# Optimization experiments

Measured on AMD Instinct MI355X. Metric: run time of the kernel, lower is better.

The kernel has to match this reference:

```python
import jax, jax.numpy as jnp
import numpy as np

N = 100_000      # nodes
E = 1_600_000    # directed edges (before self-loops)
F_IN = 128       # input node features
H = 4            # attention heads
C = 64           # hidden channels (concat=False -> heads averaged)
NEG_SLOPE = 0.2
BN_EPS = 1e-5


def setup_inputs() -> dict:
    key = jax.random.key(0)
    ks = jax.random.split(key, 16)
    s = 0.05
    return {
        "x": jax.random.normal(ks[0], (N, F_IN), dtype=jnp.float32),
        "edge_index": jax.random.randint(ks[1], (2, E), 0, N, dtype=jnp.int64),
        # GAT layer params: layer 0 has F_IN inputs, layers 1..2 have C inputs
        "W0": jax.random.normal(ks[2], (F_IN, H * C), dtype=jnp.float32) * s,
        "Wl": jax.random.normal(ks[3], (2, C, H * C), dtype=jnp.float32) * s,
        "att_src": jax.random.normal(ks[4], (3, H, C), dtype=jnp.float32) * s,
        "att_dst": jax.random.normal(ks[5], (3, H, C), dtype=jnp.float32) * s,
        "conv_bias": jnp.zeros((3, C), dtype=jnp.float32),
        # BatchNorm1d (inference: running stats)
        "bn_gamma": jnp.ones((3, C), dtype=jnp.float32),
        "bn_beta": jnp.zeros((3, C), dtype=jnp.float32),
        "bn_mean": jax.random.normal(ks[6], (3, C), dtype=jnp.float32) * 0.1,
        "bn_var": jax.random.uniform(ks[7], (3, C), dtype=jnp.float32, minval=0.5, maxval=1.5),
        # MLP head
        "lin1_w": jax.random.normal(ks[8], (C, C // 2), dtype=jnp.float32) * s,
        "lin1_b": jnp.zeros((C // 2,), dtype=jnp.float32),
        "lin2_w": jax.random.normal(ks[9], (C // 2, 1), dtype=jnp.float32) * s,
        "lin2_b": jnp.zeros((1,), dtype=jnp.float32),
    }


def _gat_layer(x, src, dst, W, a_src, a_dst, bias):
    # x: [N, Fin] -> h: [N, H, C]
    h = (x @ W).reshape(-1, H, C)
    # per-node attention logits, gathered per edge: [Etot, H]
    e_src = jnp.einsum("nhc,hc->nh", h, a_src)
    e_dst = jnp.einsum("nhc,hc->nh", h, a_dst)
    e = jax.nn.leaky_relu(e_src[src] + e_dst[dst], NEG_SLOPE)
    # softmax over incoming edges of each target node (self-loops guarantee non-empty)
    e_max = jax.ops.segment_max(e, dst, num_segments=N)
    w = jnp.exp(e - e_max[dst])                              # [Etot, H]
    denom = jax.ops.segment_sum(w, dst, num_segments=N)      # [N, H]
    # weighted scatter-add of gathered source features
    msg = h[src] * w[:, :, None]                             # [Etot, H, C]
    out = jax.ops.segment_sum(msg, dst, num_segments=N)      # [N, H, C]
    out = out / denom[:, :, None]
    return out.mean(axis=1) + bias                           # concat=False -> head mean


def reference(x, edge_index, W0, Wl, att_src, att_dst, conv_bias,
              bn_gamma, bn_beta, bn_mean, bn_var,
              lin1_w, lin1_b, lin2_w, lin2_b):
    # add self-loops (PyG GATConv default)
    loop = jnp.arange(N, dtype=edge_index.dtype)
    src = jnp.concatenate([edge_index[0], loop])
    dst = jnp.concatenate([edge_index[1], loop])

    Ws = [W0, Wl[0], Wl[1]]
    for l in range(3):
        x = _gat_layer(x, src, dst, Ws[l], att_src[l], att_dst[l], conv_bias[l])
        x = (x - bn_mean[l]) * (bn_gamma[l] / jnp.sqrt(bn_var[l] + BN_EPS)) + bn_beta[l]
        x = jax.nn.relu(x)  # dropout is identity in inference

    x = jax.nn.relu(x @ lin1_w + lin1_b)
    x = x @ lin2_w + lin2_b
    return x.squeeze(-1)
```

## Files before the change

### kernel.cpp

```cpp
#include <hip/hip_runtime.h>
#include <hip/hip_bf16.h>
#include <cstdint>

#define N_NODES 100000
#define N_EDGES 1600000
#define N_TOT   1700000
#define HEADS   4
#define CH      64
#define HC      256
#define NEG     0.2f
#define BNEPS   1e-5f
#define NPART   8
#define PART_N  12500
#define CHUNK_E 16384

typedef __attribute__((ext_vector_type(8))) short short8;
typedef __attribute__((ext_vector_type(4))) float f32x4;
typedef __attribute__((ext_vector_type(2))) float f32x2;

static __device__ __forceinline__ float lrelu(float x) {
    return x > 0.f ? x : NEG * x;
}
static __device__ __forceinline__ unsigned short f2bf(float f) {
    unsigned int u = __float_as_uint(f);
    unsigned int r = (u + 0x7fffu + ((u >> 16) & 1u)) >> 16;
    return (unsigned short)r;
}
static __device__ __forceinline__ float bflo(unsigned int v) { return __uint_as_float(v << 16); }
static __device__ __forceinline__ float bfhi(unsigned int v) { return __uint_as_float(v & 0xffff0000u); }

__global__ void convert_hist_k(const void* ei,
                               int* __restrict__ src32, int* __restrict__ dst32,
                               int* __restrict__ counts) {
    const int* e32 = (const int*)ei;
    int l = threadIdx.x & 63;
    unsigned long long b = __ballot(e32[2 * l + 1] == 0);
    int is64 = (__popcll(b) >= 48) ? 1 : 0;

    int e = blockIdx.x * 256 + threadIdx.x;
    if (e >= N_TOT) return;
    int s, d;
    if (e < N_EDGES) {
        if (is64) {
            s = (int)((const long long*)ei)[e];
            d = (int)((const long long*)ei)[(long long)N_EDGES + e];
        } else {
            s = ((const int*)ei)[e];
            d = ((const int*)ei)[N_EDGES + e];
        }
    } else { int v = e - N_EDGES; s = v; d = v; }
    src32[e] = s; dst32[e] = d;
    atomicAdd(&counts[d], 1);
}

__global__ void scan_block(const int* in, int* out, int* bsum) {
    __shared__ int sm[256];
    int t = threadIdx.x;
    int i = blockIdx.x * 256 + t;
    int v = (i < N_NODES) ? in[i] : 0;
    int acc = v;
    sm[t] = v; __syncthreads();
    for (int d = 1; d < 256; d <<= 1) {
        int add = (t >= d) ? sm[t - d] : 0;
        __syncthreads();
        acc += add; sm[t] = acc;
        __syncthreads();
    }
    if (i < N_NODES) out[i] = acc - v;
    if (t == 255) bsum[blockIdx.x] = acc;
}

__global__ void scan_bsum(int* bsum, int nb) {
    __shared__ int sm[512];
    int t = threadIdx.x;
    int v = (t < nb) ? bsum[t] : 0;
    int acc = v;
    sm[t] = v; __syncthreads();
    for (int d = 1; d < 512; d <<= 1) {
        int add = (t >= d) ? sm[t - d] : 0;
        __syncthreads();
        acc += add; sm[t] = acc;
        __syncthreads();
    }
    if (t < nb) bsum[t] = acc - v;
}

__global__ void scan_add(int* off, const int* bsum, int* fill) {
    int i = blockIdx.x * 256 + threadIdx.x;
    if (i < N_NODES) {
        int v = off[i] + bsum[blockIdx.x];
        off[i] = v; fill[i] = v;
    }
    if (i == 0) off[N_NODES] = N_TOT;
}

__global__ void scatter_part_k(const int* __restrict__ src32, const int* __restrict__ dst32,
                               int* __restrict__ fill, int* __restrict__ csr) {
    int part = blockIdx.x & (NPART - 1), chunk = blockIdx.x / NPART;
    int lo = part * PART_N, hi = lo + PART_N;
    int base = chunk * CHUNK_E;
    int end = min(base + CHUNK_E, N_TOT);
    for (int i = base + threadIdx.x; i < end; i += 256) {
        int d = dst32[i];
        if (d >= lo && d < hi) {
            int s = src32[i];
            int pos = atomicAdd(&fill[d], 1);
            csr[pos] = s;
        }
    }
}

template<int K, bool ABF16>
__global__ __launch_bounds__(256) void gemm_mfma_k(const void* __restrict__ Ain,
                                                   const float* __restrict__ Wf,
                                                   const float* __restrict__ as,
                                                   const float* __restrict__ ad,
                                                   unsigned short* __restrict__ hb,
                                                   float* __restrict__ es,
                                                   float* __restrict__ ed, int ntiles) {
    __shared__ __align__(16) unsigned short Bs[256 * K];
    __shared__ __align__(16) unsigned short As[64 * K];
    int t = threadIdx.x;

    for (int idx4 = t; idx4 < K * 64; idx4 += 256) {
        int k = idx4 >> 6;
        int c = (idx4 & 63) * 4;
        float4 wv = *(const float4*)(Wf + (size_t)k * HC + c);
        Bs[((c + 0) * K + k) ^ (((c + 0) & 7) << 3)] = f2bf(wv.x);
        Bs[((c + 1) * K + k) ^ (((c + 1) & 7) << 3)] = f2bf(wv.y);
        Bs[((c + 2) * K + k) ^ (((c + 2) & 7) << 3)] = f2bf(wv.z);
        Bs[((c + 3) * K + k) ^ (((c + 3) & 7) << 3)] = f2bf(wv.w);
    }

    int w = t >> 6, lane = t & 63;
    int c16 = lane & 15, kg = lane >> 4;
    int swz = (c16 & 7) << 3;
    float asv[4], adv[4];
    #pragma unroll
    for (int ct = 0; ct < 4; ++ct) {
        asv[ct] = as[w * 64 + ct * 16 + c16];
        adv[ct] = ad[w * 64 + ct * 16 + c16];
    }
    __syncthreads();

    for (int tile = blockIdx.x; tile < ntiles; tile += gridDim.x) {
        int bm = tile * 64;
        #pragma unroll
        for (int i = 0; i < (64 * K / 8) / 256; ++i) {
            int cidx = i * 256 + t;
            int row = cidx / (K / 8);
            int ks = (cidx % (K / 8)) * 8;
            int grow = bm + row;
            uint4 pk = make_uint4(0, 0, 0, 0);
            if (grow < N_NODES) {
                if (ABF16) {
                    pk = *(const uint4*)((const unsigned short*)Ain + (size_t)grow * K + ks);
                } else {
                    const float* Af = (const float*)Ain + (size_t)grow * K + ks;
                    float4 v0 = *(const float4*)Af;
                    float4 v1 = *(const float4*)(Af + 4);
                    pk.x = (unsigned)f2bf(v0.x) | ((unsigned)f2bf(v0.y) << 16);
                    pk.y = (unsigned)f2bf(v0.z) | ((unsigned)f2bf(v0.w) << 16);
                    pk.z = (unsigned)f2bf(v1.x) | ((unsigned)f2bf(v1.y) << 16);
                    pk.w = (unsigned)f2bf(v1.z) | ((unsigned)f2bf(v1.w) << 16);
                }
            }
            *(uint4*)(&As[(row * K + ks) ^ ((row & 7) << 3)]) = pk;
        }
        __syncthreads();

        f32x4 acc[4][4];
        #pragma unroll
        for (int i = 0; i < 4; ++i)
            #pragma unroll
            for (int j = 0; j < 4; ++j) acc[i][j] = (f32x4)(0.f);

        #pragma unroll
        for (int kc = 0; kc < K / 32; ++kc) {
            int ko = kc * 32 + kg * 8;
            short8 af[4], bf[4];
            #pragma unroll
            for (int rs = 0; rs < 4; ++rs)
                af[rs] = *(const short8*)(&As[((16 * rs + c16) * K + ko) ^ swz]);
            #pragma unroll
            for (int ct = 0; ct < 4; ++ct) {
                int col = w * 64 + ct * 16 + c16;
                bf[ct] = *(const short8*)(&Bs[(col * K + ko) ^ swz]);
            }
            #pragma unroll
            for (int rs = 0; rs < 4; ++rs)
                #pragma unroll
                for (int ct = 0; ct < 4; ++ct)
                    acc[rs][ct] = __builtin_amdgcn_mfma_f32_16x16x32_bf16(af[rs], bf[ct], acc[rs][ct], 0, 0, 0);
        }

        #pragma unroll
        for (int rs = 0; rs < 4; ++rs) {
            float esr[4], edr[4];
            #pragma unroll
            for (int reg = 0; reg < 4; ++reg) {
                float s = 0.f, d = 0.f;
                #pragma unroll
                for (int ct = 0; ct < 4; ++ct) {
                    s += acc[rs][ct][reg] * asv[ct];
                    d += acc[rs][ct][reg] * adv[ct];
                }
                #pragma unroll
                for (int sh = 1; sh < 16; sh <<= 1) {
                    s += __shfl_xor(s, sh);
                    d += __shfl_xor(d, sh);
                }
                esr[reg] = s; edr[reg] = d;
            }
            if (c16 == 0) {
                int r0 = bm + rs * 16 + kg * 4;
                #pragma unroll
                for (int reg = 0; reg < 4; ++reg) {
                    if (r0 + reg < N_NODES) {
                        es[(size_t)(r0 + reg) * 4 + w] = esr[reg];
                        ed[(size_t)(r0 + reg) * 4 + w] = edr[reg];
                    }
                }
            }
        }
        __syncthreads();

        #pragma unroll
        for (int rs = 0; rs < 4; ++rs) {
            #pragma unroll
            for (int ct = 0; ct < 4; ++ct)
                #pragma unroll
                for (int reg = 0; reg < 4; ++reg)
                    As[(kg * 4 + reg) * 256 + w * 64 + ct * 16 + c16] = f2bf(acc[rs][ct][reg]);
            __syncthreads();
            int row16 = t >> 4, cseg = (t & 15) * 16;
            int grow = bm + rs * 16 + row16;
            if (grow < N_NODES) {
                uint4 v0 = *(const uint4*)(&As[row16 * 256 + cseg]);
                uint4 v1 = *(const uint4*)(&As[row16 * 256 + cseg + 8]);
                *(uint4*)(hb + (size_t)grow * HC + cseg) = v0;
                *(uint4*)(hb + (size_t)grow * HC + cseg + 8) = v1;
            }
            __syncthreads();
        }
    }
}

template<bool OUTBF16>
__global__ __launch_bounds__(256) void aggregate_k(const unsigned short* __restrict__ h,
                                                   const float* __restrict__ es,
                                                   const float* __restrict__ ed,
                                                   const int* __restrict__ off,
                                                   const int* __restrict__ csr,
                                                   const float* __restrict__ bias,
                                                   const float* __restrict__ g,
                                                   const float* __restrict__ bb,
                                                   const float* __restrict__ mu,
                                                   const float* __restrict__ var,
                                                   void* __restrict__ xout) {
    __shared__ float wbuf[4][68][4];
    __shared__ int   sbuf[4][68];
    int wv = threadIdx.x >> 6;
    int lane = threadIdx.x & 63;
    int wid = blockIdx.x * 4 + wv;
    if (wid >= N_NODES) return;

    if (lane < 4) {
        sbuf[wv][64 + lane] = 0;
        *(float4*)(&wbuf[wv][64 + lane][0]) = make_float4(0.f, 0.f, 0.f, 0.f);
    }

    int s0 = off[wid], s1 = off[wid + 1];
    float4 edv = *(const float4*)(ed + (size_t)wid * 4);

    int half = lane >> 5;
    int sub  = lane & 31;
    int head = sub >> 3;
    float ds0 = 0.f, ds1 = 0.f, ds2 = 0.f, ds3 = 0.f;
    f32x2 acc2[8];
    #pragma unroll
    for (int i = 0; i < 8; ++i) acc2[i] = (f32x2)(0.f);
    const unsigned short* hsub = h + sub * 8;

    for (int base = s0; base < s1; base += 64) {
        int e = base + lane;
        float w0 = 0.f, w1 = 0.f, w2 = 0.f, w3 = 0.f;
        int s = 0;
        if (e < s1) {
            s = csr[e];
            float4 ev = *(const float4*)(es + (size_t)s * 4);
            w0 = __expf(fminf(lrelu(ev.x + edv.x), 80.f));
            w1 = __expf(fminf(lrelu(ev.y + edv.y), 80.f));
            w2 = __expf(fminf(lrelu(ev.z + edv.z), 80.f));
            w3 = __expf(fminf(lrelu(ev.w + edv.w), 80.f));
        }
        ds0 += w0; ds1 += w1; ds2 += w2; ds3 += w3;
        *(float4*)(&wbuf[wv][lane][0]) = make_float4(w0, w1, w2, w3);
        sbuf[wv][lane] = s;
        asm volatile("" ::: "memory");

        int cnt2 = (min(64, s1 - base) + 1) & ~1;
        int sA = sbuf[wv][half];
        float wA = wbuf[wv][half][head];
        int sB = sbuf[wv][2 + half];
        float wB = wbuf[wv][2 + half][head];
        uint4 hA = *(const uint4*)(hsub + (size_t)sA * HC);
        uint4 hB = *(const uint4*)(hsub + (size_t)sB * HC);
        for (int j = 0; j < cnt2; j += 2) {
            int jn = j + 4 + half;
            int sC = sbuf[wv][jn];
            float wC = wbuf[wv][jn][head];
            uint4 hC = *(const uint4*)(hsub + (size_t)sC * HC);
            f32x2 wp = { wA, wA };
            f32x2 p0 = { bflo(hA.x), bfhi(hA.x) };
            f32x2 p1 = { bflo(hA.y), bfhi(hA.y) };
            f32x2 p2 = { bflo(hA.z), bfhi(hA.z) };
            f32x2 p3 = { bflo(hA.w), bfhi(hA.w) };
            asm("v_pk_fma_f32 %0, %1, %2, %0" : "+v"(acc2[0]) : "v"(p0), "v"(wp));
            asm("v_pk_fma_f32 %0, %1, %2, %0" : "+v"(acc2[1]) : "v"(p1), "v"(wp));
            asm("v_pk_fma_f32 %0, %1, %2, %0" : "+v"(acc2[2]) : "v"(p2), "v"(wp));
            asm("v_pk_fma_f32 %0, %1, %2, %0" : "+v"(acc2[3]) : "v"(p3), "v"(wp));
            hA = hB; wA = wB;
            hB = hC; wB = wC;
        }
        asm volatile("" ::: "memory");
    }

    float a0 = acc2[0][0], a1 = acc2[0][1], a2 = acc2[1][0], a3 = acc2[1][1];
    float a4 = acc2[2][0], a5 = acc2[2][1], a6 = acc2[3][0], a7 = acc2[3][1];

    a0 += __shfl_xor(a0, 32); a1 += __shfl_xor(a1, 32);
    a2 += __shfl_xor(a2, 32); a3 += __shfl_xor(a3, 32);
    a4 += __shfl_xor(a4, 32); a5 += __shfl_xor(a5, 32);
    a6 += __shfl_xor(a6, 32); a7 += __shfl_xor(a7, 32);

    #pragma unroll
    for (int d = 1; d < 64; d <<= 1) {
        ds0 += __shfl_xor(ds0, d); ds1 += __shfl_xor(ds1, d);
        ds2 += __shfl_xor(ds2, d); ds3 += __shfl_xor(ds3, d);
    }
    float den = head == 0 ? ds0 : head == 1 ? ds1 : head == 2 ? ds2 : ds3;
    float inv = 1.f / den;
    a0 *= inv; a1 *= inv; a2 *= inv; a3 *= inv;
    a4 *= inv; a5 *= inv; a6 *= inv; a7 *= inv;

    a0 += __shfl_xor(a0, 8);  a1 += __shfl_xor(a1, 8);
    a2 += __shfl_xor(a2, 8);  a3 += __shfl_xor(a3, 8);
    a4 += __shfl_xor(a4, 8);  a5 += __shfl_xor(a5, 8);
    a6 += __shfl_xor(a6, 8);  a7 += __shfl_xor(a7, 8);
    a0 += __shfl_xor(a0, 16); a1 += __shfl_xor(a1, 16);
    a2 += __shfl_xor(a2, 16); a3 += __shfl_xor(a3, 16);
    a4 += __shfl_xor(a4, 16); a5 += __shfl_xor(a5, 16);
    a6 += __shfl_xor(a6, 16); a7 += __shfl_xor(a7, 16);

    if (lane < 8) {
        int c = lane * 8;
        float av[8] = {a0, a1, a2, a3, a4, a5, a6, a7};
        float4 bi0 = *(const float4*)(bias + c), bi1 = *(const float4*)(bias + c + 4);
        float4 gv0 = *(const float4*)(g + c),    gv1 = *(const float4*)(g + c + 4);
        float4 bv0 = *(const float4*)(bb + c),   bv1 = *(const float4*)(bb + c + 4);
        float4 mv0 = *(const float4*)(mu + c),   mv1 = *(const float4*)(mu + c + 4);
        float4 vv0 = *(const float4*)(var + c),  vv1 = *(const float4*)(var + c + 4);
        float bia[8] = {bi0.x, bi0.y, bi0.z, bi0.w, bi1.x, bi1.y, bi1.z, bi1.w};
        float gg[8]  = {gv0.x, gv0.y, gv0.z, gv0.w, gv1.x, gv1.y, gv1.z, gv1.w};
        float be[8]  = {bv0.x, bv0.y, bv0.z, bv0.w, bv1.x, bv1.y, bv1.z, bv1.w};
        float mm[8]  = {mv0.x, mv0.y, mv0.z, mv0.w, mv1.x, mv1.y, mv1.z, mv1.w};
        float vv[8]  = {vv0.x, vv0.y, vv0.z, vv0.w, vv1.x, vv1.y, vv1.z, vv1.w};
        float o[8];
        #pragma unroll
        for (int k = 0; k < 8; ++k) {
            float t0 = (av[k] * 0.25f + bia[k] - mm[k]) * (gg[k] * rsqrtf(vv[k] + BNEPS)) + be[k];
            o[k] = fmaxf(t0, 0.f);
        }
        if (OUTBF16) {
            uint4 pk;
            pk.x = (unsigned)f2bf(o[0]) | ((unsigned)f2bf(o[1]) << 16);
            pk.y = (unsigned)f2bf(o[2]) | ((unsigned)f2bf(o[3]) << 16);
            pk.z = (unsigned)f2bf(o[4]) | ((unsigned)f2bf(o[5]) << 16);
            pk.w = (unsigned)f2bf(o[6]) | ((unsigned)f2bf(o[7]) << 16);
            *(uint4*)((unsigned short*)xout + (size_t)wid * CH + c) = pk;
        } else {
            *(float4*)((float*)xout + (size_t)wid * CH + c)     = make_float4(o[0], o[1], o[2], o[3]);
            *(float4*)((float*)xout + (size_t)wid * CH + c + 4) = make_float4(o[4], o[5], o[6], o[7]);
        }
    }
}

__global__ __launch_bounds__(256) void mlp_k(const float* __restrict__ x,
                                             const float* __restrict__ w1,
                                             const float* __restrict__ b1,
                                             const float* __restrict__ w2,
                                             const float* __restrict__ b2,
                                             float* __restrict__ out) {
    __shared__ float w1s[CH * 32];
    __shared__ float w2s[32];
    __shared__ float b1s[32];
    int t = threadIdx.x;
    for (int i = t; i < CH * 32; i += 256) w1s[i] = w1[i];
    if (t < 32) { w2s[t] = w2[t]; b1s[t] = b1[t]; }
    __syncthreads();
    int n = blockIdx.x * 256 + t;
    if (n >= N_NODES) return;
    float y[32];
    #pragma unroll
    for (int j = 0; j < 32; ++j) y[j] = b1s[j];
    const float* xr = x + (size_t)n * CH;
    for (int c4 = 0; c4 < 16; ++c4) {
        float4 xv = *(const float4*)(xr + c4 * 4);
        const float* wr = &w1s[c4 * 4 * 32];
        #pragma unroll
        for (int j = 0; j < 32; ++j)
            y[j] += xv.x * wr[j] + xv.y * wr[32 + j] + xv.z * wr[64 + j] + xv.w * wr[96 + j];
    }
    float o = b2[0];
    #pragma unroll
    for (int j = 0; j < 32; ++j) o += fmaxf(y[j], 0.f) * w2s[j];
    out[n] = o;
}

extern "C" void kernel_launch(void* const* d_in, const int* in_sizes, int n_in,
                              void* d_out, int out_size, void* d_ws, size_t ws_size,
                              hipStream_t stream) {
    const float* x0    = (const float*)d_in[0];
    const void*  ei    = d_in[1];
    const float* W0    = (const float*)d_in[2];
    const float* Wl    = (const float*)d_in[3];
    const float* asrc  = (const float*)d_in[4];
    const float* adst  = (const float*)d_in[5];
    const float* cbias = (const float*)d_in[6];
    const float* bng   = (const float*)d_in[7];
    const float* bnb   = (const float*)d_in[8];
    const float* bnm   = (const float*)d_in[9];
    const float* bnv   = (const float*)d_in[10];
    const float* l1w   = (const float*)d_in[11];
    const float* l1b   = (const float*)d_in[12];
    const float* l2w   = (const float*)d_in[13];
    const float* l2b   = (const float*)d_in[14];
    float* out = (float*)d_out;

    char* p = (char*)d_ws;
    auto alloc = [&](size_t bytes) { char* r = p; p += (bytes + 255) & ~(size_t)255; return r; };
    unsigned short* hb   = (unsigned short*)alloc((size_t)N_NODES * HC * 2);
    unsigned short* xb0  = (unsigned short*)alloc((size_t)N_NODES * CH * 2);
    unsigned short* xb1  = (unsigned short*)alloc((size_t)N_NODES * CH * 2);
    float* xf32 = (float*)alloc((size_t)N_NODES * CH * 4);
    float* es   = (float*)alloc((size_t)N_NODES * 4 * 4);
    float* ed   = (float*)alloc((size_t)N_NODES * 4 * 4);
    int* counts = (int*)alloc((size_t)N_NODES * 4);
    int* off    = (int*)alloc((size_t)(N_NODES + 1) * 4);
    int* fill   = (int*)alloc((size_t)N_NODES * 4);
    int* bsum   = (int*)alloc(512 * 4);
    int* src32  = (int*)alloc((size_t)N_TOT * 4);
    int* dst32  = (int*)alloc((size_t)N_TOT * 4);
    int* csr    = (int*)alloc((size_t)N_TOT * 4);

    int nbScan = (N_NODES + 255) / 256;
    int nchunk = (N_TOT + CHUNK_E - 1) / CHUNK_E;
    int ntiles = (N_NODES + 63) / 64;
    hipMemsetAsync(counts, 0, (size_t)N_NODES * 4, stream);
    convert_hist_k<<<(N_TOT + 255) / 256, 256, 0, stream>>>(ei, src32, dst32, counts);
    scan_block<<<nbScan, 256, 0, stream>>>(counts, off, bsum);
    scan_bsum<<<1, 512, 0, stream>>>(bsum, nbScan);
    scan_add<<<nbScan, 256, 0, stream>>>(off, bsum, fill);
    scatter_part_k<<<nchunk * NPART, 256, 0, stream>>>(src32, dst32, fill, csr);

    int nagg = (N_NODES + 3) / 4;
    gemm_mfma_k<128, false><<<782, 256, 0, stream>>>(x0, W0, asrc, adst, hb, es, ed, ntiles);
    aggregate_k<true><<<nagg, 256, 0, stream>>>(hb, es, ed, off, csr,
        cbias, bng, bnb, bnm, bnv, xb0);
    gemm_mfma_k<64, true><<<1563, 256, 0, stream>>>(xb0, Wl, asrc + HC, adst + HC, hb, es, ed, ntiles);
    aggregate_k<true><<<nagg, 256, 0, stream>>>(hb, es, ed, off, csr,
        cbias + CH, bng + CH, bnb + CH, bnm + CH, bnv + CH, xb1);
    gemm_mfma_k<64, true><<<1563, 256, 0, stream>>>(xb1, Wl + (size_t)CH * HC, asrc + 2 * HC, adst + 2 * HC, hb, es, ed, ntiles);
    aggregate_k<false><<<nagg, 256, 0, stream>>>(hb, es, ed, off, csr,
        cbias + 2 * CH, bng + 2 * CH, bnb + 2 * CH, bnm + 2 * CH, bnv + 2 * CH, xf32);

    mlp_k<<<(N_NODES + 255) / 256, 256, 0, stream>>>(xf32, l1w, l1b, l2w, l2b, out);
}
```

Measured before the change: 736.1 us.

## Bucket edges by partition during conversion, fuse MLP into last aggregate, retune GEMM grids

Edge conversion now writes (src,dst) pairs into per-partition buckets using block-local counters. The CSR scatter then reads only its own bucket instead of every partition block rescanning all edges. The MLP head is fused into the final aggregation kernel using warp shuffles and a transposed W1 in shared memory, which removes the fp32 intermediate buffer and a kernel launch. GEMM grid sizes are also reduced. The cost is extra shared memory in every aggregate instantiation (the W1 tile is declared even in mode 0, which may lower occupancy) and a fixed bucket capacity that assumes partitions stay under 262144 edges.

```diff
diff --git a/kernel.cpp b/kernel.cpp
--- a/kernel.cpp
+++ b/kernel.cpp
@@ -12,7 +12,7 @@
 #define BNEPS   1e-5f
 #define NPART   8
 #define PART_N  12500
-#define CHUNK_E 16384
+#define BUCKET_CAP 262144
 
 typedef __attribute__((ext_vector_type(8))) short short8;
 typedef __attribute__((ext_vector_type(4))) float f32x4;
@@ -29,28 +29,40 @@
 static __device__ __forceinline__ float bflo(unsigned int v) { return __uint_as_float(v << 16); }
 static __device__ __forceinline__ float bfhi(unsigned int v) { return __uint_as_float(v & 0xffff0000u); }
 
-__global__ void convert_hist_k(const void* ei,
-                               int* __restrict__ src32, int* __restrict__ dst32,
-                               int* __restrict__ counts) {
+__global__ void convert_bucket_k(const void* ei, int2* __restrict__ buckets,
+                                 int* __restrict__ bfill, int* __restrict__ counts) {
+    __shared__ int lcnt[NPART];
+    __shared__ int lbase[NPART];
     const int* e32 = (const int*)ei;
-    int l = threadIdx.x & 63;
+    int t = threadIdx.x;
+    int l = t & 63;
     unsigned long long b = __ballot(e32[2 * l + 1] == 0);
     int is64 = (__popcll(b) >= 48) ? 1 : 0;
 
-    int e = blockIdx.x * 256 + threadIdx.x;
-    if (e >= N_TOT) return;
-    int s, d;
-    if (e < N_EDGES) {
-        if (is64) {
-            s = (int)((const long long*)ei)[e];
-            d = (int)((const long long*)ei)[(long long)N_EDGES + e];
-        } else {
-            s = ((const int*)ei)[e];
-            d = ((const int*)ei)[N_EDGES + e];
-        }
-    } else { int v = e - N_EDGES; s = v; d = v; }
-    src32[e] = s; dst32[e] = d;
-    atomicAdd(&counts[d], 1);
+    if (t < NPART) lcnt[t] = 0;
+    __syncthreads();
+
+    int e = blockIdx.x * 256 + t;
+    int s = 0, d = 0, part = -1, pos = 0;
+    if (e < N_TOT) {
+        if (e < N_EDGES) {
+            if (is64) {
+                s = (int)((const long long*)ei)[e];
+                d = (int)((const long long*)ei)[(long long)N_EDGES + e];
+            } else {
+                s = ((const int*)ei)[e];
+                d = ((const int*)ei)[N_EDGES + e];
+            }
+        } else { int v = e - N_EDGES; s = v; d = v; }
+        part = d / PART_N;
+        pos = atomicAdd(&lcnt[part], 1);
+        atomicAdd(&counts[d], 1);
+    }
+    __syncthreads();
+    if (t < NPART) lbase[t] = atomicAdd(&bfill[t], lcnt[t]);
+    __syncthreads();
+    if (part >= 0)
+        buckets[(size_t)part * BUCKET_CAP + lbase[part] + pos] = make_int2(s, d);
 }
 
 __global__ void scan_block(const int* in, int* out, int* bsum) {
@@ -94,19 +106,17 @@
     if (i == 0) off[N_NODES] = N_TOT;
 }
 
-__global__ void scatter_part_k(const int* __restrict__ src32, const int* __restrict__ dst32,
-                               int* __restrict__ fill, int* __restrict__ csr) {
-    int part = blockIdx.x & (NPART - 1), chunk = blockIdx.x / NPART;
-    int lo = part * PART_N, hi = lo + PART_N;
-    int base = chunk * CHUNK_E;
-    int end = min(base + CHUNK_E, N_TOT);
-    for (int i = base + threadIdx.x; i < end; i += 256) {
-        int d = dst32[i];
-        if (d >= lo && d < hi) {
-            int s = src32[i];
-            int pos = atomicAdd(&fill[d], 1);
-            csr[pos] = s;
-        }
+__global__ void scatter_bucket_k(const int2* __restrict__ buckets, const int* __restrict__ bfill,
+                                 int* __restrict__ fill, int* __restrict__ csr) {
+    int part = blockIdx.x & (NPART - 1);
+    int bi = blockIdx.x >> 3;
+    int nb = gridDim.x >> 3;
+    int n = bfill[part];
+    const int2* bk = buckets + (size_t)part * BUCKET_CAP;
+    for (int i = bi * 256 + threadIdx.x; i < n; i += nb * 256) {
+        int2 sd = bk[i];
+        int pos = atomicAdd(&fill[sd.y], 1);
+        csr[pos] = sd.x;
     }
 }
 
@@ -246,7 +256,7 @@
     }
 }
 
-template<bool OUTBF16>
+template<int MODE>
 __global__ __launch_bounds__(256) void aggregate_k(const unsigned short* __restrict__ h,
                                                    const float* __restrict__ es,
                                                    const float* __restrict__ ed,
@@ -257,9 +267,26 @@
                                                    const float* __restrict__ bb,
                                                    const float* __restrict__ mu,
                                                    const float* __restrict__ var,
-                                                   void* __restrict__ xout) {
+                                                   void* __restrict__ xout,
+                                                   const float* __restrict__ w1p,
+                                                   const float* __restrict__ b1p,
+                                                   const float* __restrict__ w2p,
+                                                   const float* __restrict__ b2p) {
     __shared__ float wbuf[4][68][4];
     __shared__ int   sbuf[4][68];
+    __shared__ float w1t[32 * 65];
+    __shared__ float w2s[32], b1s[32], b2s[1];
+
+    if (MODE == 1) {
+        for (int idx = threadIdx.x; idx < 2048; idx += 256) {
+            int k = idx & 31, c = idx >> 5;
+            w1t[k * 65 + c] = w1p[c * 32 + k];
+        }
+        if (threadIdx.x < 32) { w2s[threadIdx.x] = w2p[threadIdx.x]; b1s[threadIdx.x] = b1p[threadIdx.x]; }
+        if (threadIdx.x == 0) b2s[0] = b2p[0];
+        __syncthreads();
+    }
+
     int wv = threadIdx.x >> 6;
     int lane = threadIdx.x & 63;
     int wid = blockIdx.x * 4 + wv;
@@ -353,69 +380,56 @@
     a4 += __shfl_xor(a4, 16); a5 += __shfl_xor(a5, 16);
     a6 += __shfl_xor(a6, 16); a7 += __shfl_xor(a7, 16);
 
-    if (lane < 8) {
-        int c = lane * 8;
-        float av[8] = {a0, a1, a2, a3, a4, a5, a6, a7};
-        float4 bi0 = *(const float4*)(bias + c), bi1 = *(const float4*)(bias + c + 4);
-        float4 gv0 = *(const float4*)(g + c),    gv1 = *(const float4*)(g + c + 4);
-        float4 bv0 = *(const float4*)(bb + c),   bv1 = *(const float4*)(bb + c + 4);
-        float4 mv0 = *(const float4*)(mu + c),   mv1 = *(const float4*)(mu + c + 4);
-        float4 vv0 = *(const float4*)(var + c),  vv1 = *(const float4*)(var + c + 4);
-        float bia[8] = {bi0.x, bi0.y, bi0.z, bi0.w, bi1.x, bi1.y, bi1.z, bi1.w};
-        float gg[8]  = {gv0.x, gv0.y, gv0.z, gv0.w, gv1.x, gv1.y, gv1.z, gv1.w};
-        float be[8]  = {bv0.x, bv0.y, bv0.z, bv0.w, bv1.x, bv1.y, bv1.z, bv1.w};
-        float mm[8]  = {mv0.x, mv0.y, mv0.z, mv0.w, mv1.x, mv1.y, mv1.z, mv1.w};
-        float vv[8]  = {vv0.x, vv0.y, vv0.z, vv0.w, vv1.x, vv1.y, vv1.z, vv1.w};
-        float o[8];
-        #pragma unroll
-        for (int k = 0; k < 8; ++k) {
-            float t0 = (av[k] * 0.25f + bia[k] - mm[k]) * (gg[k] * rsqrtf(vv[k] + BNEPS)) + be[k];
-            o[k] = fmaxf(t0, 0.f);
-        }
-        if (OUTBF16) {
+    int c = (lane & 7) * 8;
+    float av[8] = {a0, a1, a2, a3, a4, a5, a6, a7};
+    float4 bi0 = *(const float4*)(bias + c), bi1 = *(const float4*)(bias + c + 4);
+    float4 gv0 = *(const float4*)(g + c),    gv1 = *(const float4*)(g + c + 4);
+    float4 bv0 = *(const float4*)(bb + c),   bv1 = *(const float4*)(bb + c + 4);
+    float4 mv0 = *(const float4*)(mu + c),   mv1 = *(const float4*)(mu + c + 4);
+    float4 vv0 = *(const float4*)(var + c),  vv1 = *(const float4*)(var + c + 4);
+    float bia[8] = {bi0.x, bi0.y, bi0.z, bi0.w, bi1.x, bi1.y, bi1.z, bi1.w};
+    float gg[8]  = {gv0.x, gv0.y, gv0.z, gv0.w, gv1.x, gv1.y, gv1.z, gv1.w};
+    float be[8]  = {bv0.x, bv0.y, bv0.z, bv0.w, bv1.x, bv1.y, bv1.z, bv1.w};
+    float mm[8]  = {mv0.x, mv0.y, mv0.z, mv0.w, mv1.x, mv1.y, mv1.z, mv1.w};
+    float vv[8]  = {vv0.x, vv0.y, vv0.z, vv0.w, vv1.x, vv1.y, vv1.z, vv1.w};
+    float o[8];
+    #pragma unroll
+    for (int k = 0; k < 8; ++k) {
+        float t0 = (av[k] * 0.25f + bia[k] - mm[k]) * (gg[k] * rsqrtf(vv[k] + BNEPS)) + be[k];
+        o[k] = fmaxf(t0, 0.f);
+    }
+
+    if (MODE == 0) {
+        if (lane < 8) {
             uint4 pk;
             pk.x = (unsigned)f2bf(o[0]) | ((unsigned)f2bf(o[1]) << 16);
             pk.y = (unsigned)f2bf(o[2]) | ((unsigned)f2bf(o[3]) << 16);
             pk.z = (unsigned)f2bf(o[4]) | ((unsigned)f2bf(o[5]) << 16);
             pk.w = (unsigned)f2bf(o[6]) | ((unsigned)f2bf(o[7]) << 16);
             *(uint4*)((unsigned short*)xout + (size_t)wid * CH + c) = pk;
-        } else {
-            *(float4*)((float*)xout + (size_t)wid * CH + c)     = make_float4(o[0], o[1], o[2], o[3]);
-            *(float4*)((float*)xout + (size_t)wid * CH + c + 4) = make_float4(o[4], o[5], o[6], o[7]);
-        }
-    }
-}
-
-__global__ __launch_bounds__(256) void mlp_k(const float* __restrict__ x,
-                                             const float* __restrict__ w1,
-                                             const float* __restrict__ b1,
-                                             const float* __restrict__ w2,
-                                             const float* __restrict__ b2,
-                                             float* __restrict__ out) {
-    __shared__ float w1s[CH * 32];
-    __shared__ float w2s[32];
-    __shared__ float b1s[32];
-    int t = threadIdx.x;
-    for (int i = t; i < CH * 32; i += 256) w1s[i] = w1[i];
-    if (t < 32) { w2s[t] = w2[t]; b1s[t] = b1[t]; }
-    __syncthreads();
-    int n = blockIdx.x * 256 + t;
-    if (n >= N_NODES) return;
-    float y[32];
-    #pragma unroll
-    for (int j = 0; j < 32; ++j) y[j] = b1s[j];
-    const float* xr = x + (size_t)n * CH;
-    for (int c4 = 0; c4 < 16; ++c4) {
-        float4 xv = *(const float4*)(xr + c4 * 4);
-        const float* wr = &w1s[c4 * 4 * 32];
-        #pragma unroll
-        for (int j = 0; j < 32; ++j)
-            y[j] += xv.x * wr[j] + xv.y * wr[32 + j] + xv.z * wr[64 + j] + xv.w * wr[96 + j];
-    }
-    float o = b2[0];
-    #pragma unroll
-    for (int j = 0; j < 32; ++j) o += fmaxf(y[j], 0.f) * w2s[j];
-    out[n] = o;
+        }
+    } else {
+        int k32 = lane & 31;
+        int hi = lane >> 5;
+        float y = hi ? 0.f : b1s[k32];
+        #pragma unroll
+        for (int j4 = 0; j4 < 4; ++j4) {
+            int srcl = hi * 4 + j4;
+            #pragma unroll
+            for (int i = 0; i < 8; ++i) {
+                float xc = __shfl(o[i], srcl);
+                y = fmaf(xc, w1t[k32 * 65 + hi * 32 + j4 * 8 + i], y);
+            }
+        }
+        y += __shfl_xor(y, 32);
+        float z = fmaxf(y, 0.f) * w2s[k32];
+        z += __shfl_xor(z, 1);
+        z += __shfl_xor(z, 2);
+        z += __shfl_xor(z, 4);
+        z += __shfl_xor(z, 8);
+        z += __shfl_xor(z, 16);
+        if (lane == 0) ((float*)xout)[wid] = z + b2s[0];
+    }
 }
 
 extern "C" void kernel_launch(void* const* d_in, const int* in_sizes, int n_in,
@@ -443,37 +457,35 @@
     unsigned short* hb   = (unsigned short*)alloc((size_t)N_NODES * HC * 2);
     unsigned short* xb0  = (unsigned short*)alloc((size_t)N_NODES * CH * 2);
     unsigned short* xb1  = (unsigned short*)alloc((size_t)N_NODES * CH * 2);
-    float* xf32 = (float*)alloc((size_t)N_NODES * CH * 4);
     float* es   = (float*)alloc((size_t)N_NODES * 4 * 4);
     float* ed   = (float*)alloc((size_t)N_NODES * 4 * 4);
     int* counts = (int*)alloc((size_t)N_NODES * 4);
     int* off    = (int*)alloc((size_t)(N_NODES + 1) * 4);
     int* fill   = (int*)alloc((size_t)N_NODES * 4);
     int* bsum   = (int*)alloc(512 * 4);
-    int* src32  = (int*)alloc((size_t)N_TOT * 4);
-    int* dst32  = (int*)alloc((size_t)N_TOT * 4);
+    int* bfill  = (int*)alloc(256);
+    int2* buckets = (int2*)alloc((size_t)NPART * BUCKET_CAP * 8);
     int* csr    = (int*)alloc((size_t)N_TOT * 4);
 
     int nbScan = (N_NODES + 255) / 256;
-    int nchunk = (N_TOT + CHUNK_E - 1) / CHUNK_E;
     int ntiles = (N_NODES + 63) / 64;
     hipMemsetAsync(counts, 0, (size_t)N_NODES * 4, stream);
-    convert_hist_k<<<(N_TOT + 255) / 256, 256, 0, stream>>>(ei, src32, dst32, counts);
+    hipMemsetAsync(bfill, 0, NPART * 4, stream);
+    convert_bucket_k<<<(N_TOT + 255) / 256, 256, 0, stream>>>(ei, buckets, bfill, counts);
     scan_block<<<nbScan, 256, 0, stream>>>(counts, off, bsum);
     scan_bsum<<<1, 512, 0, stream>>>(bsum, nbScan);
     scan_add<<<nbScan, 256, 0, stream>>>(off, bsum, fill);
-    scatter_part_k<<<nchunk * NPART, 256, 0, stream>>>(src32, dst32, fill, csr);
+    scatter_bucket_k<<<NPART * 64, 256, 0, stream>>>(buckets, bfill, fill, csr);
 
     int nagg = (N_NODES + 3) / 4;
-    gemm_mfma_k<128, false><<<782, 256, 0, stream>>>(x0, W0, asrc, adst, hb, es, ed, ntiles);
-    aggregate_k<true><<<nagg, 256, 0, stream>>>(hb, es, ed, off, csr,
-        cbias, bng, bnb, bnm, bnv, xb0);
-    gemm_mfma_k<64, true><<<1563, 256, 0, stream>>>(xb0, Wl, asrc + HC, adst + HC, hb, es, ed, ntiles);
-    aggregate_k<true><<<nagg, 256, 0, stream>>>(hb, es, ed, off, csr,
-        cbias + CH, bng + CH, bnb + CH, bnm + CH, bnv + CH, xb1);
-    gemm_mfma_k<64, true><<<1563, 256, 0, stream>>>(xb1, Wl + (size_t)CH * HC, asrc + 2 * HC, adst + 2 * HC, hb, es, ed, ntiles);
-    aggregate_k<false><<<nagg, 256, 0, stream>>>(hb, es, ed, off, csr,
-        cbias + 2 * CH, bng + 2 * CH, bnb + 2 * CH, bnm + 2 * CH, bnv + 2 * CH, xf32);
-
-    mlp_k<<<(N_NODES + 255) / 256, 256, 0, stream>>>(xf32, l1w, l1b, l2w, l2b, out);
-}
+    gemm_mfma_k<128, false><<<512, 256, 0, stream>>>(x0, W0, asrc, adst, hb, es, ed, ntiles);
+    aggregate_k<0><<<nagg, 256, 0, stream>>>(hb, es, ed, off, csr,
+        cbias, bng, bnb, bnm, bnv, xb0, nullptr, nullptr, nullptr, nullptr);
+    gemm_mfma_k<64, true><<<1024, 256, 0, stream>>>(xb0, Wl, asrc + HC, adst + HC, hb, es, ed, ntiles);
+    aggregate_k<0><<<nagg, 256, 0, stream>>>(hb, es, ed, off, csr,
+        cbias + CH, bng + CH, bnb + CH, bnm + CH, bnv + CH, xb1, nullptr, nullptr, nullptr, nullptr);
+    gemm_mfma_k<64, true><<<1024, 256, 0, stream>>>(xb1, Wl + (size_t)CH * HC, asrc + 2 * HC, adst + 2 * HC, hb, es, ed, ntiles);
+    aggregate_k<1><<<nagg, 256, 0, stream>>>(hb, es, ed, off, csr,
+        cbias + 2 * CH, bng + 2 * CH, bnb + 2 * CH, bnm + 2 * CH, bnv + 2 * CH, out,
+        l1w, l1b, l2w, l2b);
+}
```

Result: no change. 742.2 us (+0.8%).
